# Kernel tuning notes

Hardware: AMD Instinct MI355X
Metric: run time of the kernel (lower is better)

## Reference

```python
import jax, jax.numpy as jnp
import numpy as np

N_NODES = 50000
N_EDGES = 800000
N_GRAPHS = 128
D = 128
L = 4
C = 10
GN_EPS = 1e-5


def setup_inputs() -> dict:
    key = jax.random.key(0)
    ks = jax.random.split(key, 12)
    s = 0.05
    x = jax.random.normal(ks[0], (N_NODES, D), dtype=jnp.float32)
    gin_w1 = jax.random.normal(ks[1], (L, D, D), dtype=jnp.float32) * s
    gin_b1 = jax.random.normal(ks[2], (L, D), dtype=jnp.float32) * s
    gin_w2 = jax.random.normal(ks[3], (L, D, D), dtype=jnp.float32) * s
    gin_b2 = jax.random.normal(ks[4], (L, D), dtype=jnp.float32) * s
    gn_weight = jnp.ones((L, D), dtype=jnp.float32)
    gn_bias = jnp.zeros((L, D), dtype=jnp.float32)
    gn_scale = jnp.ones((L, D), dtype=jnp.float32)
    fw1 = jax.random.normal(ks[5], (D, D), dtype=jnp.float32) * s
    fb1 = jnp.zeros((D,), dtype=jnp.float32)
    fw2 = jax.random.normal(ks[6], (D, D), dtype=jnp.float32) * s
    fb2 = jnp.zeros((D,), dtype=jnp.float32)
    fw3 = jax.random.normal(ks[7], (D, C), dtype=jnp.float32) * s
    fb3 = jnp.zeros((C,), dtype=jnp.float32)
    edge_index = jax.random.randint(ks[8], (2, N_EDGES), 0, N_NODES, dtype=jnp.int64)
    batch = jnp.sort(jax.random.randint(ks[9], (N_NODES,), 0, N_GRAPHS, dtype=jnp.int64))
    return dict(x=x, gin_w1=gin_w1, gin_b1=gin_b1, gin_w2=gin_w2, gin_b2=gin_b2,
                gn_weight=gn_weight, gn_bias=gn_bias, gn_scale=gn_scale,
                fw1=fw1, fb1=fb1, fw2=fw2, fb2=fb2, fw3=fw3, fb3=fb3,
                edge_index=edge_index, batch=batch)


def _graph_norm(h, batch, weight, bias, mean_scale, counts):
    # PyG GraphNorm: per-graph mean/var with learnable mean_scale.
    mean = jax.ops.segment_sum(h, batch, num_segments=N_GRAPHS) / counts  # [G, D]
    out = h - mean[batch] * mean_scale
    var = jax.ops.segment_sum(out * out, batch, num_segments=N_GRAPHS) / counts
    return weight * out / jnp.sqrt(var[batch] + GN_EPS) + bias


def reference(x, gin_w1, gin_b1, gin_w2, gin_b2, gn_weight, gn_bias, gn_scale,
              fw1, fb1, fw2, fb2, fw3, fb3, edge_index, batch):
    src, dst = edge_index[0], edge_index[1]
    ones = jnp.ones((N_NODES, 1), dtype=x.dtype)
    counts = jnp.maximum(jax.ops.segment_sum(ones, batch, num_segments=N_GRAPHS), 1.0)  # [G,1]
    h = x
    for l in range(L):
        # GINConv, eps=0: (1+eps)*x + sum_{j->i} x_j, then MLP with act after each Linear
        agg = jax.ops.segment_sum(h[src], dst, num_segments=N_NODES)  # [N, D]
        h = h + agg
        h = jax.nn.relu(h @ gin_w1[l] + gin_b1[l])
        h = jax.nn.relu(h @ gin_w2[l] + gin_b2[l])
        h = _graph_norm(h, batch, gn_weight[l], gn_bias[l], gn_scale[l], counts)
        h = jax.nn.relu(h)
    # sum readout per graph
    g = jax.ops.segment_sum(h, batch, num_segments=N_GRAPHS)  # [G, D]
    # final MLP (dropout is identity in eval)
    g = jax.nn.relu(g @ fw1 + fb1)
    g = jax.nn.relu(g @ fw2 + fb2)
    out = g @ fw3 + fb3
    return jax.nn.log_softmax(out, axis=-1)
```

## Files before the change

### kernel.cpp

```cpp
#include <hip/hip_runtime.h>
#include <cstddef>

#define N_NODES 50000
#define N_EDGES 800000
#define N_GRAPHS 128
#define DIM 128
#define N_LAYERS 4
#define GN_EPS 1e-5f

#define B_CHUNK 256
#define EPB 3125
#define BUCKET_SHIFT 9
#define BUCKET_SIZE 512
#define NB 98
#define SCAN_BLKS 25

#define CX_BLKS 3125
#define CW_BLKS 512
#define GB_BLKS 196
#define SETUP_BLKS (CX_BLKS + CW_BLKS + GB_BLKS + B_CHUNK)

typedef unsigned short ushort_t;
typedef __attribute__((ext_vector_type(8))) short frag8;
typedef __attribute__((ext_vector_type(4))) float f32x4;

__device__ inline float bfbits2f(unsigned hi16) { return __uint_as_float(hi16 << 16); }
__device__ inline ushort_t bf16rne(float v) {
    unsigned u = __float_as_uint(v);
    unsigned r = u + 0x7fff + ((u >> 16) & 1);
    return (ushort_t)(r >> 16);
}
__device__ inline unsigned packbf2(float a, float b) {
    return (unsigned)bf16rne(a) | ((unsigned)bf16rne(b) << 16);
}
__device__ inline void bf16split(float v, ushort_t& h, ushort_t& l) {
    ushort_t hi = bf16rne(v);
    float fh = __uint_as_float(((unsigned)hi) << 16);
    l = bf16rne(v - fh);
    h = hi;
}

__global__ __launch_bounds__(256) void setup_misc(const float4* __restrict__ x4, uint4* __restrict__ Hb4,
                                                  const float* __restrict__ w1, const float* __restrict__ w2,
                                                  ushort_t* __restrict__ whi, ushort_t* __restrict__ wlo,
                                                  const int* __restrict__ batch, int* __restrict__ gstart,
                                                  const int* __restrict__ edst, int* __restrict__ cnts) {
    __shared__ int cnt[NB];
    int b = blockIdx.x, t = threadIdx.x;
    if (b < CX_BLKS) {
        int i = b * 256 + t;
        if (i < N_NODES * 16) {
            float4 a = x4[2 * i], bb = x4[2 * i + 1];
            uint4 o;
            o.x = packbf2(a.x, a.y);
            o.y = packbf2(a.z, a.w);
            o.z = packbf2(bb.x, bb.y);
            o.w = packbf2(bb.z, bb.w);
            Hb4[i] = o;
        }
    } else if (b < CX_BLKS + CW_BLKS) {
        int idx = (b - CX_BLKS) * 256 + t;
        int mat = idx >> 14;
        int e = idx & 16383;
        int n = e >> 7, k = e & 127;
        int l = mat >> 1;
        const float* src = (mat & 1) ? (w2 + (size_t)l * DIM * DIM) : (w1 + (size_t)l * DIM * DIM);
        float v = src[k * DIM + n];
        ushort_t h, lw;
        bf16split(v, h, lw);
        whi[(size_t)mat * DIM * DIM + n * DIM + k] = h;
        wlo[(size_t)mat * DIM * DIM + n * DIM + k] = lw;
    } else if (b < CX_BLKS + CW_BLKS + GB_BLKS) {
        int i = (b - CX_BLKS - CW_BLKS) * 256 + t;
        if (i < N_NODES) {
            int bb = batch[i];
            if (i == 0) {
                for (int g = 0; g <= bb; ++g) gstart[g] = 0;
            } else {
                int pb = batch[i - 1];
                for (int g = pb + 1; g <= bb; ++g) gstart[g] = i;
            }
            if (i == N_NODES - 1) {
                for (int g = bb + 1; g <= N_GRAPHS; ++g) gstart[g] = N_NODES;
            }
        }
    } else {
        int blk = b - (CX_BLKS + CW_BLKS + GB_BLKS);
        for (int i = t; i < NB; i += 256) cnt[i] = 0;
        __syncthreads();
        int base = blk * EPB;
        for (int i = t; i < EPB; i += 256) atomicAdd(&cnt[edst[base + i] >> BUCKET_SHIFT], 1);
        __syncthreads();
        for (int i = t; i < NB; i += 256) cnts[i * B_CHUNK + blk] = cnt[i];
    }
}

__global__ __launch_bounds__(1024) void scan_local(const int* __restrict__ in, int* __restrict__ out,
                                                   int* __restrict__ bsum, int n) {
    __shared__ int wsum[16];
    int tid = threadIdx.x, lane = tid & 63, w = tid >> 6;
    int gi = blockIdx.x * 1024 + tid;
    int v = (gi < n) ? in[gi] : 0;
    int s = v;
    #pragma unroll
    for (int off = 1; off < 64; off <<= 1) {
        int t = __shfl_up(s, off, 64);
        if (lane >= off) s += t;
    }
    if (lane == 63) wsum[w] = s;
    __syncthreads();
    if (w == 0) {
        int ws = (lane < 16) ? wsum[lane] : 0;
        #pragma unroll
        for (int off = 1; off < 16; off <<= 1) {
            int t = __shfl_up(ws, off, 64);
            if (lane >= off) ws += t;
        }
        if (lane < 16) wsum[lane] = ws;
    }
    __syncthreads();
    int woff = (w > 0) ? wsum[w - 1] : 0;
    if (gi < n) out[gi] = woff + s - v;
    if (tid == 1023) bsum[blockIdx.x] = woff + s;
}

__global__ __launch_bounds__(256) void p3_place(const int* __restrict__ src, const int* __restrict__ dst,
                                                const int* __restrict__ off, const int* __restrict__ bsum,
                                                unsigned* __restrict__ ebuf) {
    __shared__ int cur[NB];
    __shared__ int pexc[32];
    int t = threadIdx.x, blk = blockIdx.x;
    if (t < 32) {
        int v = (t < SCAN_BLKS) ? bsum[t] : 0;
        int sI = v;
        #pragma unroll
        for (int o = 1; o < 32; o <<= 1) {
            int u = __shfl_up(sI, o, 64);
            if (t >= o) sI += u;
        }
        pexc[t] = sI - v;
    }
    __syncthreads();
    for (int i = t; i < NB; i += 256) {
        int j = i * B_CHUNK + blk;
        cur[i] = off[j] + pexc[j >> 10];
    }
    __syncthreads();
    int base = blk * EPB;
    for (int i = t; i < EPB; i += 256) {
        int d = dst[base + i];
        int b = d >> BUCKET_SHIFT;
        int pos = atomicAdd(&cur[b], 1);
        ebuf[pos] = (unsigned)src[base + i] | ((unsigned)(d & (BUCKET_SIZE - 1)) << 16);
    }
}

__global__ __launch_bounds__(512) void p4_csr(const unsigned* __restrict__ ebuf, const int* __restrict__ off,
                                              const int* __restrict__ bsum,
                                              int* __restrict__ eoff, int* __restrict__ csr) {
    __shared__ int cnt[BUCKET_SIZE];
    __shared__ int wsum[8];
    __shared__ int pexc[32];
    int k = blockIdx.x, t = threadIdx.x;
    if (t < 32) {
        int v = (t < SCAN_BLKS) ? bsum[t] : 0;
        int sI = v;
        #pragma unroll
        for (int o = 1; o < 32; o <<= 1) {
            int u = __shfl_up(sI, o, 64);
            if (t >= o) sI += u;
        }
        pexc[t] = sI - v;
    }
    cnt[t] = 0;
    __syncthreads();
    int bstart = off[k * B_CHUNK] + pexc[(k * B_CHUNK) >> 10];
    int bend = (k == NB - 1) ? N_EDGES
                             : off[(k + 1) * B_CHUNK] + pexc[((k + 1) * B_CHUNK) >> 10];
    for (int i = bstart + t; i < bend; i += 512) atomicAdd(&cnt[ebuf[i] >> 16], 1);
    __syncthreads();
    int lane = t & 63, w = t >> 6;
    int v = cnt[t], s = v;
    #pragma unroll
    for (int o = 1; o < 64; o <<= 1) {
        int tt = __shfl_up(s, o, 64);
        if (lane >= o) s += tt;
    }
    if (lane == 63) wsum[w] = s;
    __syncthreads();
    if (w == 0) {
        int ws = (lane < 8) ? wsum[lane] : 0;
        #pragma unroll
        for (int o = 1; o < 8; o <<= 1) {
            int tt = __shfl_up(ws, o, 64);
            if (lane >= o) ws += tt;
        }
        if (lane < 8) wsum[lane] = ws;
    }
    __syncthreads();
    int woff = (w > 0) ? wsum[w - 1] : 0;
    int excl = woff + s - v;
    int node = k * BUCKET_SIZE + t;
    if (node < N_NODES) eoff[node] = bstart + excl;
    __syncthreads();
    cnt[t] = excl;
    __syncthreads();
    for (int i = bstart + t; i < bend; i += 512) {
        unsigned p = ebuf[i];
        int pos = atomicAdd(&cnt[p >> 16], 1);
        csr[bstart + pos] = (int)(p & 0xffffu);
    }
    if (k == NB - 1 && t == 0) eoff[N_NODES] = N_EDGES;
}

__global__ __launch_bounds__(256) void agg_bf16(const uint4* __restrict__ h4, const int* __restrict__ eoff,
                                                const int* __restrict__ csr, uint4* __restrict__ T4) {
    int wid = (blockIdx.x * 256 + threadIdx.x) >> 6;
    int lane = threadIdx.x & 63;
    int qtr = lane >> 4;
    int ql = lane & 15;
    if (wid >= N_NODES) return;
    int lo = eoff[wid], hi = eoff[wid + 1];

    float a[8];
    #pragma unroll
    for (int k = 0; k < 8; ++k) a[k] = 0.f;

    auto acc_row = [&](uint4 w) {
        a[0] += bfbits2f(w.x & 0xffffu); a[1] += bfbits2f(w.x >> 16);
        a[2] += bfbits2f(w.y & 0xffffu); a[3] += bfbits2f(w.y >> 16);
        a[4] += bfbits2f(w.z & 0xffffu); a[5] += bfbits2f(w.z >> 16);
        a[6] += bfbits2f(w.w & 0xffffu); a[7] += bfbits2f(w.w >> 16);
    };

    if (qtr == 0) acc_row(h4[(size_t)wid * 16 + ql]);

    for (int base = lo; base < hi; base += 64) {
        int nav = hi - base;
        if (nav > 64) nav = 64;
        int jv = (base + lane < hi) ? csr[base + lane] : 0;
        int cmin = nav >> 2;
        int cmax = (nav + 3) >> 2;
        int i = 0;
        for (; i + 3 < cmin; i += 4) {
            int j0 = __shfl(jv, 4 * (i + 0) + qtr, 64);
            int j1 = __shfl(jv, 4 * (i + 1) + qtr, 64);
            int j2 = __shfl(jv, 4 * (i + 2) + qtr, 64);
            int j3 = __shfl(jv, 4 * (i + 3) + qtr, 64);
            uint4 w0 = h4[(size_t)j0 * 16 + ql];
            uint4 w1 = h4[(size_t)j1 * 16 + ql];
            uint4 w2 = h4[(size_t)j2 * 16 + ql];
            uint4 w3 = h4[(size_t)j3 * 16 + ql];
            acc_row(w0); acc_row(w1); acc_row(w2); acc_row(w3);
        }
        for (; i < cmin; ++i) {
            int j = __shfl(jv, 4 * i + qtr, 64);
            acc_row(h4[(size_t)j * 16 + ql]);
        }
        for (; i < cmax; ++i) {
            int epos = 4 * i + qtr;
            int j = __shfl(jv, epos, 64);
            if (epos < nav) acc_row(h4[(size_t)j * 16 + ql]);
        }
    }

    #pragma unroll
    for (int k = 0; k < 8; ++k) {
        a[k] += __shfl_down(a[k], 32, 64);
        a[k] += __shfl_down(a[k], 16, 64);
    }
    if (qtr == 0) {
        uint4 o;
        o.x = packbf2(a[0], a[1]);
        o.y = packbf2(a[2], a[3]);
        o.z = packbf2(a[4], a[5]);
        o.w = packbf2(a[6], a[7]);
        T4[(size_t)wid * 16 + ql] = o;
    }
}

__global__ __launch_bounds__(512) void mm_layer(const ushort_t* __restrict__ A,
                                                const ushort_t* __restrict__ W1h, const ushort_t* __restrict__ W1l,
                                                const ushort_t* __restrict__ W2h, const ushort_t* __restrict__ W2l,
                                                const float* __restrict__ b1, const float* __restrict__ b2,
                                                ushort_t* __restrict__ Zb) {
    __shared__ ushort_t As[256 * 128];
    __shared__ ushort_t Ws[128 * 128];
    int tid = threadIdx.x;
    int row0 = blockIdx.x * 256;
    int wave = tid >> 6, lane = tid & 63;
    int q = lane >> 4, mn = lane & 15;

    f32x4 acc[2][8];
    #pragma unroll
    for (int t = 0; t < 2; ++t)
        #pragma unroll
        for (int n = 0; n < 8; ++n) acc[t][n] = (f32x4)(0.f);

    #pragma unroll
    for (int i = 0; i < 8; ++i) {
        int c = tid + i * 512;
        int r = c >> 4, c8 = c & 15;
        uint4 v = make_uint4(0u, 0u, 0u, 0u);
        int gr = row0 + r;
        if (gr < N_NODES) v = *(const uint4*)(A + (size_t)gr * DIM + c8 * 8);
        *(uint4*)(&As[r * 128 + (c8 ^ (r & 7)) * 8]) = v;
    }
    auto stageW = [&](const ushort_t* src) {
        #pragma unroll
        for (int i = 0; i < 4; ++i) {
            int c = tid + i * 512;
            int r = c >> 4, c8 = c & 15;
            uint4 v = *(const uint4*)(src + r * DIM + c8 * 8);
            *(uint4*)(&Ws[r * 128 + (c8 ^ (r & 7)) * 8]) = v;
        }
    };
    auto compute = [&]() {
        #pragma unroll
        for (int ks = 0; ks < 4; ++ks) {
            int m0 = wave * 32 + mn;
            int m1 = m0 + 16;
            frag8 a0 = *(const frag8*)&As[m0 * 128 + (((ks * 4 + q) ^ (m0 & 7)) * 8)];
            frag8 a1 = *(const frag8*)&As[m1 * 128 + (((ks * 4 + q) ^ (m1 & 7)) * 8)];
            #pragma unroll
            for (int n = 0; n < 8; ++n) {
                int nr = n * 16 + mn;
                frag8 b = *(const frag8*)&Ws[nr * 128 + (((ks * 4 + q) ^ (nr & 7)) * 8)];
                acc[0][n] = __builtin_amdgcn_mfma_f32_16x16x32_bf16(a0, b, acc[0][n], 0, 0, 0);
                acc[1][n] = __builtin_amdgcn_mfma_f32_16x16x32_bf16(a1, b, acc[1][n], 0, 0, 0);
            }
        }
    };

    stageW(W1h);
    __syncthreads(); compute(); __syncthreads();
    stageW(W1l);
    __syncthreads(); compute(); __syncthreads();

    int mloc = wave * 32;
    #pragma unroll
    for (int t = 0; t < 2; ++t) {
        #pragma unroll
        for (int n = 0; n < 8; ++n) {
            int col = n * 16 + mn;
            float bv = b1[col];
            #pragma unroll
            for (int r = 0; r < 4; ++r) {
                int rloc = mloc + t * 16 + q * 4 + r;
                float v = fmaxf(acc[t][n][r] + bv, 0.f);
                As[rloc * 128 + ((col >> 3) ^ (rloc & 7)) * 8 + (col & 7)] = bf16rne(v);
                acc[t][n][r] = 0.f;
            }
        }
    }
    __syncthreads();
    stageW(W2h);
    __syncthreads(); compute(); __syncthreads();
    stageW(W2l);
    __syncthreads(); compute();

    #pragma unroll
    for (int t = 0; t < 2; ++t) {
        #pragma unroll
        for (int n = 0; n < 8; ++n) {
            int col = n * 16 + mn;
            float bv = b2[col];
            #pragma unroll
            for (int r = 0; r < 4; ++r) {
                int grow = row0 + mloc + t * 16 + q * 4 + r;
                if (grow < N_NODES)
                    Zb[(size_t)grow * DIM + col] = bf16rne(fmaxf(acc[t][n][r] + bv, 0.f));
            }
        }
    }
}

__global__ __launch_bounds__(1024) void gn_fused(const unsigned* __restrict__ Zb, const int* __restrict__ gstart,
                                                 const float* __restrict__ scale, const float* __restrict__ weight,
                                                 const float* __restrict__ bias,
                                                 unsigned* __restrict__ Hb) {
    __shared__ f32x4 sh1[1024], sh2[1024];
    __shared__ float sa[64], sb[64];
    int g = blockIdx.x >> 1, half = blockIdx.x & 1;
    int t = threadIdx.x;
    int uld = t & 15, rg = t >> 4;
    int s = gstart[g], e = gstart[g + 1];
    const unsigned* zp = Zb + half * 32 + uld * 2;
    f32x4 s1 = (f32x4)(0.f), s2 = (f32x4)(0.f);
    for (int n = s + rg; n < e; n += 64) {
        uint2 zz = *(const uint2*)(zp + (size_t)n * 64);
        f32x4 z;
        z[0] = bfbits2f(zz.x & 0xffffu); z[1] = bfbits2f(zz.x >> 16);
        z[2] = bfbits2f(zz.y & 0xffffu); z[3] = bfbits2f(zz.y >> 16);
        s1 += z;
        s2 += z * z;
    }
    sh1[t] = s1;
    sh2[t] = s2;
    __syncthreads();
    int dbase = half * 64 + uld * 4;
    if (rg == 0) {
        #pragma unroll 8
        for (int k = 1; k < 64; ++k) { s1 += sh1[uld + 16 * k]; s2 += sh2[uld + 16 * k]; }
        int cnt = e - s;
        float cf = (float)(cnt > 0 ? cnt : 1);
        #pragma unroll
        for (int j = 0; j < 4; ++j) {
            float m = s1[j] / cf, ez = s2[j] / cf;
            float sc = scale[dbase + j];
            float var = fmaxf(ez - (2.0f - sc) * sc * m * m, 0.f);
            sa[uld * 4 + j] = m * sc;
            sb[uld * 4 + j] = weight[dbase + j] / sqrtf(var + GN_EPS);
        }
    }
    __syncthreads();
    float as0 = sa[uld * 4], as1 = sa[uld * 4 + 1], as2 = sa[uld * 4 + 2], as3 = sa[uld * 4 + 3];
    float bm0 = sb[uld * 4], bm1 = sb[uld * 4 + 1], bm2 = sb[uld * 4 + 2], bm3 = sb[uld * 4 + 3];
    float bi0 = bias[dbase], bi1 = bias[dbase + 1], bi2 = bias[dbase + 2], bi3 = bias[dbase + 3];
    unsigned* hp = Hb + half * 32 + uld * 2;
    for (int n = s + rg; n < e; n += 64) {
        uint2 zz = *(const uint2*)(zp + (size_t)n * 64);
        float z0 = bfbits2f(zz.x & 0xffffu), z1 = bfbits2f(zz.x >> 16);
        float z2 = bfbits2f(zz.y & 0xffffu), z3 = bfbits2f(zz.y >> 16);
        float o0 = fmaxf((z0 - as0) * bm0 + bi0, 0.f);
        float o1 = fmaxf((z1 - as1) * bm1 + bi1, 0.f);
        float o2 = fmaxf((z2 - as2) * bm2 + bi2, 0.f);
        float o3 = fmaxf((z3 - as3) * bm3 + bi3, 0.f);
        uint2 o;
        o.x = packbf2(o0, o1);
        o.y = packbf2(o2, o3);
        *(uint2*)(hp + (size_t)n * 64) = o;
    }
}

__global__ __launch_bounds__(1024) void gn_last(const unsigned* __restrict__ Zb, const int* __restrict__ gstart,
                                                const float* __restrict__ scale, const float* __restrict__ weight,
                                                const float* __restrict__ bias,
                                                const float* __restrict__ fw1, const float* __restrict__ fb1,
                                                const float* __restrict__ fw2, const float* __restrict__ fb2,
                                                const float* __restrict__ fw3, const float* __restrict__ fb3,
                                                float* __restrict__ out) {
    __shared__ f32x4 sh1[1024], sh2[1024];
    __shared__ float sa[128], sb[128];
    __shared__ float v0[128], v1[128], v2[128], lg[10];
    int g = blockIdx.x;
    int t = threadIdx.x;
    int du = t & 31, rg = t >> 5;
    int s = gstart[g], e = gstart[g + 1];
    const unsigned* zp = Zb + du * 2;
    f32x4 s1 = (f32x4)(0.f), s2 = (f32x4)(0.f);
    for (int n = s + rg; n < e; n += 32) {
        uint2 zz = *(const uint2*)(zp + (size_t)n * 64);
        f32x4 z;
        z[0] = bfbits2f(zz.x & 0xffffu); z[1] = bfbits2f(zz.x >> 16);
        z[2] = bfbits2f(zz.y & 0xffffu); z[3] = bfbits2f(zz.y >> 16);
        s1 += z;
        s2 += z * z;
    }
    sh1[t] = s1;
    sh2[t] = s2;
    __syncthreads();
    int dbase = du * 4;
    if (rg == 0) {
        #pragma unroll 8
        for (int k = 1; k < 32; ++k) { s1 += sh1[du + 32 * k]; s2 += sh2[du + 32 * k]; }
        int cnt = e - s;
        float cf = (float)(cnt > 0 ? cnt : 1);
        #pragma unroll
        for (int j = 0; j < 4; ++j) {
            float m = s1[j] / cf, ez = s2[j] / cf;
            float sc = scale[dbase + j];
            float var = fmaxf(ez - (2.0f - sc) * sc * m * m, 0.f);
            sa[dbase + j] = m * sc;
            sb[dbase + j] = weight[dbase + j] / sqrtf(var + GN_EPS);
        }
    }
    __syncthreads();
    float as_[4], bm_[4], bi_[4];
    #pragma unroll
    for (int j = 0; j < 4; ++j) {
        as_[j] = sa[dbase + j];
        bm_[j] = sb[dbase + j];
        bi_[j] = bias[dbase + j];
    }
    f32x4 rsum = (f32x4)(0.f);
    for (int n = s + rg; n < e; n += 32) {
        uint2 zz = *(const uint2*)(zp + (size_t)n * 64);
        float z0 = bfbits2f(zz.x & 0xffffu), z1 = bfbits2f(zz.x >> 16);
        float z2 = bfbits2f(zz.y & 0xffffu), z3 = bfbits2f(zz.y >> 16);
        rsum[0] += fmaxf((z0 - as_[0]) * bm_[0] + bi_[0], 0.f);
        rsum[1] += fmaxf((z1 - as_[1]) * bm_[1] + bi_[1], 0.f);
        rsum[2] += fmaxf((z2 - as_[2]) * bm_[2] + bi_[2], 0.f);
        rsum[3] += fmaxf((z3 - as_[3]) * bm_[3] + bi_[3], 0.f);
    }
    __syncthreads();
    sh1[t] = rsum;
    __syncthreads();
    if (rg == 0) {
        #pragma unroll 8
        for (int k = 1; k < 32; ++k) rsum += sh1[du + 32 * k];
        #pragma unroll
        for (int j = 0; j < 4; ++j) v0[dbase + j] = rsum[j];
    }
    __syncthreads();
    if (t < 128) {
        float acc = fb1[t];
        for (int d = 0; d < 128; ++d) acc += v0[d] * fw1[d * 128 + t];
        v1[t] = fmaxf(acc, 0.f);
    }
    __syncthreads();
    if (t < 128) {
        float acc = fb2[t];
        for (int d = 0; d < 128; ++d) acc += v1[d] * fw2[d * 128 + t];
        v2[t] = fmaxf(acc, 0.f);
    }
    __syncthreads();
    if (t < 10) {
        float acc = fb3[t];
        for (int d = 0; d < 128; ++d) acc += v2[d] * fw3[d * 10 + t];
        lg[t] = acc;
    }
    __syncthreads();
    if (t < 10) {
        float m = -1e30f;
        for (int c = 0; c < 10; ++c) m = fmaxf(m, lg[c]);
        float ssum = 0.f;
        for (int c = 0; c < 10; ++c) ssum += expf(lg[c] - m);
        out[g * 10 + t] = lg[t] - m - logf(ssum);
    }
}

extern "C" void kernel_launch(void* const* d_in, const int* in_sizes, int n_in,
                              void* d_out, int out_size, void* d_ws, size_t ws_size,
                              hipStream_t stream) {
    const float* x      = (const float*)d_in[0];
    const float* gin_w1 = (const float*)d_in[1];
    const float* gin_b1 = (const float*)d_in[2];
    const float* gin_w2 = (const float*)d_in[3];
    const float* gin_b2 = (const float*)d_in[4];
    const float* gn_w   = (const float*)d_in[5];
    const float* gn_b   = (const float*)d_in[6];
    const float* gn_s   = (const float*)d_in[7];
    const float* fw1    = (const float*)d_in[8];
    const float* fb1    = (const float*)d_in[9];
    const float* fw2    = (const float*)d_in[10];
    const float* fb2    = (const float*)d_in[11];
    const float* fw3    = (const float*)d_in[12];
    const float* fb3    = (const float*)d_in[13];
    const int*   eidx   = (const int*)d_in[14];
    const int*   batch  = (const int*)d_in[15];
    float* out = (float*)d_out;

    const int* esrc = eidx;
    const int* edst = eidx + N_EDGES;

    auto align_up = [](size_t v) { return (v + 255) & ~(size_t)255; };
    char* p = (char*)d_ws;
    unsigned* Hb = (unsigned*)p;   p += align_up((size_t)N_NODES * DIM * 2);
    unsigned* Tb = (unsigned*)p;   p += align_up((size_t)N_NODES * DIM * 2);
    unsigned* Zb = (unsigned*)p;   p += align_up((size_t)N_NODES * DIM * 2);
    ushort_t* WThi = (ushort_t*)p; p += align_up((size_t)8 * DIM * DIM * 2);
    ushort_t* WTlo = (ushort_t*)p; p += align_up((size_t)8 * DIM * DIM * 2);
    int* gstart = (int*)p;         p += align_up((N_GRAPHS + 1) * 4);
    int* cnts = (int*)p;           p += align_up((size_t)NB * B_CHUNK * 4);
    int* off = (int*)p;            p += align_up(((size_t)NB * B_CHUNK + 1) * 4);
    int* bsum = (int*)p;           p += align_up(64 * 4);
    unsigned* ebuf = (unsigned*)p; p += align_up((size_t)N_EDGES * 4);
    int* eoff = (int*)p;           p += align_up((N_NODES + 1) * 4);
    int* csr = (int*)p;            p += align_up((size_t)N_EDGES * 4);

    const int SCAN_N = NB * B_CHUNK;
    setup_misc<<<SETUP_BLKS, 256, 0, stream>>>((const float4*)x, (uint4*)Hb, gin_w1, gin_w2,
                                               WThi, WTlo, batch, gstart, edst, cnts);
    scan_local<<<SCAN_BLKS, 1024, 0, stream>>>(cnts, off, bsum, SCAN_N);
    p3_place<<<B_CHUNK, 256, 0, stream>>>(esrc, edst, off, bsum, ebuf);
    p4_csr<<<NB, 512, 0, stream>>>(ebuf, off, bsum, eoff, csr);

    const int mm_grid = (N_NODES + 255) / 256;
    for (int l = 0; l < N_LAYERS; ++l) {
        agg_bf16<<<(N_NODES + 3) / 4, 256, 0, stream>>>((const uint4*)Hb, eoff, csr, (uint4*)Tb);
        mm_layer<<<mm_grid, 512, 0, stream>>>((const ushort_t*)Tb,
            WThi + (size_t)(2 * l) * DIM * DIM, WTlo + (size_t)(2 * l) * DIM * DIM,
            WThi + (size_t)(2 * l + 1) * DIM * DIM, WTlo + (size_t)(2 * l + 1) * DIM * DIM,
            gin_b1 + l * DIM, gin_b2 + l * DIM, (ushort_t*)Zb);
        if (l == N_LAYERS - 1)
            gn_last<<<N_GRAPHS, 1024, 0, stream>>>(Zb, gstart, gn_s + l * DIM,
                gn_w + l * DIM, gn_b + l * DIM, fw1, fb1, fw2, fb2, fw3, fb3, out);
        else
            gn_fused<<<N_GRAPHS * 2, 1024, 0, stream>>>(Zb, gstart, gn_s + l * DIM,
                gn_w + l * DIM, gn_b + l * DIM, Hb);
    }
}
```

Baseline: 380.9 us.

## Double-buffer weight staging in mm_layer and use packed float2 accumulation in agg

The MLP kernel gets two LDS buffers for weight tiles, so loading the low-half weights overlaps the MFMA compute on the high half, and fewer barriers are needed per layer. The aggregation kernel now accumulates bf16 pairs into float2 vectors so the compiler can emit packed adds. The second buffer adds 32KB of LDS per block, which may lower occupancy of the matmul kernel.

```diff
diff --git a/kernel.cpp b/kernel.cpp
--- a/kernel.cpp
+++ b/kernel.cpp
@@ -23,6 +23,7 @@
 typedef unsigned short ushort_t;
 typedef __attribute__((ext_vector_type(8))) short frag8;
 typedef __attribute__((ext_vector_type(4))) float f32x4;
+typedef __attribute__((ext_vector_type(2))) float f32x2;
 
 __device__ inline float bfbits2f(unsigned hi16) { return __uint_as_float(hi16 << 16); }
 __device__ inline ushort_t bf16rne(float v) {
@@ -38,6 +39,12 @@
     float fh = __uint_as_float(((unsigned)hi) << 16);
     l = bf16rne(v - fh);
     h = hi;
+}
+__device__ inline f32x2 bf2pair(unsigned w) {
+    union { unsigned u[2]; f32x2 f; } c;
+    c.u[0] = w << 16;
+    c.u[1] = w & 0xffff0000u;
+    return c.f;
 }
 
 __global__ __launch_bounds__(256) void setup_misc(const float4* __restrict__ x4, uint4* __restrict__ Hb4,
@@ -222,15 +229,15 @@
     if (wid >= N_NODES) return;
     int lo = eoff[wid], hi = eoff[wid + 1];
 
-    float a[8];
-    #pragma unroll
-    for (int k = 0; k < 8; ++k) a[k] = 0.f;
+    f32x2 a[4];
+    #pragma unroll
+    for (int k = 0; k < 4; ++k) a[k] = (f32x2)(0.f);
 
     auto acc_row = [&](uint4 w) {
-        a[0] += bfbits2f(w.x & 0xffffu); a[1] += bfbits2f(w.x >> 16);
-        a[2] += bfbits2f(w.y & 0xffffu); a[3] += bfbits2f(w.y >> 16);
-        a[4] += bfbits2f(w.z & 0xffffu); a[5] += bfbits2f(w.z >> 16);
-        a[6] += bfbits2f(w.w & 0xffffu); a[7] += bfbits2f(w.w >> 16);
+        a[0] += bf2pair(w.x);
+        a[1] += bf2pair(w.y);
+        a[2] += bf2pair(w.z);
+        a[3] += bf2pair(w.w);
     };
 
     if (qtr == 0) acc_row(h4[(size_t)wid * 16 + ql]);
@@ -264,17 +271,18 @@
         }
     }
 
+    float f[8] = {a[0].x, a[0].y, a[1].x, a[1].y, a[2].x, a[2].y, a[3].x, a[3].y};
     #pragma unroll
     for (int k = 0; k < 8; ++k) {
-        a[k] += __shfl_down(a[k], 32, 64);
-        a[k] += __shfl_down(a[k], 16, 64);
+        f[k] += __shfl_down(f[k], 32, 64);
+        f[k] += __shfl_down(f[k], 16, 64);
     }
     if (qtr == 0) {
         uint4 o;
-        o.x = packbf2(a[0], a[1]);
-        o.y = packbf2(a[2], a[3]);
-        o.z = packbf2(a[4], a[5]);
-        o.w = packbf2(a[6], a[7]);
+        o.x = packbf2(f[0], f[1]);
+        o.y = packbf2(f[2], f[3]);
+        o.z = packbf2(f[4], f[5]);
+        o.w = packbf2(f[6], f[7]);
         T4[(size_t)wid * 16 + ql] = o;
     }
 }
@@ -285,7 +293,7 @@
                                                 const float* __restrict__ b1, const float* __restrict__ b2,
                                                 ushort_t* __restrict__ Zb) {
     __shared__ ushort_t As[256 * 128];
-    __shared__ ushort_t Ws[128 * 128];
+    __shared__ ushort_t Ws[2][128 * 128];
     int tid = threadIdx.x;
     int row0 = blockIdx.x * 256;
     int wave = tid >> 6, lane = tid & 63;
@@ -306,16 +314,16 @@
         if (gr < N_NODES) v = *(const uint4*)(A + (size_t)gr * DIM + c8 * 8);
         *(uint4*)(&As[r * 128 + (c8 ^ (r & 7)) * 8]) = v;
     }
-    auto stageW = [&](const ushort_t* src) {
+    auto stageW = [&](int buf, const ushort_t* src) {
         #pragma unroll
         for (int i = 0; i < 4; ++i) {
             int c = tid + i * 512;
             int r = c >> 4, c8 = c & 15;
             uint4 v = *(const uint4*)(src + r * DIM + c8 * 8);
-            *(uint4*)(&Ws[r * 128 + (c8 ^ (r & 7)) * 8]) = v;
+            *(uint4*)(&Ws[buf][r * 128 + (c8 ^ (r & 7)) * 8]) = v;
         }
     };
-    auto compute = [&]() {
+    auto compute = [&](int buf) {
         #pragma unroll
         for (int ks = 0; ks < 4; ++ks) {
             int m0 = wave * 32 + mn;
@@ -325,17 +333,20 @@
             #pragma unroll
             for (int n = 0; n < 8; ++n) {
                 int nr = n * 16 + mn;
-                frag8 b = *(const frag8*)&Ws[nr * 128 + (((ks * 4 + q) ^ (nr & 7)) * 8)];
+                frag8 b = *(const frag8*)&Ws[buf][nr * 128 + (((ks * 4 + q) ^ (nr & 7)) * 8)];
                 acc[0][n] = __builtin_amdgcn_mfma_f32_16x16x32_bf16(a0, b, acc[0][n], 0, 0, 0);
                 acc[1][n] = __builtin_amdgcn_mfma_f32_16x16x32_bf16(a1, b, acc[1][n], 0, 0, 0);
             }
         }
     };
 
-    stageW(W1h);
-    __syncthreads(); compute(); __syncthreads();
-    stageW(W1l);
-    __syncthreads(); compute(); __syncthreads();
+    stageW(0, W1h);
+    __syncthreads();
+    stageW(1, W1l);
+    compute(0);
+    __syncthreads();
+    compute(1);
+    __syncthreads();
 
     int mloc = wave * 32;
     #pragma unroll
@@ -353,11 +364,13 @@
             }
         }
     }
-    __syncthreads();
-    stageW(W2h);
-    __syncthreads(); compute(); __syncthreads();
-    stageW(W2l);
-    __syncthreads(); compute();
+    stageW(0, W2h);
+    __syncthreads();
+
+    stageW(1, W2l);
+    compute(0);
+    __syncthreads();
+    compute(1);
 
     #pragma unroll
     for (int t = 0; t < 2; ++t) {
```

Measured after the change: 381.6 us (median of 2 runs). About the same (+0.2%).
